# Optimization experiments

Hardware: AMD Instinct MI355X
Metric: run time of the kernel (lower is better)

Reference implementation:

```python
import jax, jax.numpy as jnp
import numpy as np

MAX_LEN = 128
VOCAB = 32000
SENTINEL = 2**30  # larger than any valid token id; pushes masked slots to the end after sort


def setup_inputs() -> dict:
    key = jax.random.key(0)
    k1, k2, k3, k4 = jax.random.split(key, 4)
    B, L = 262144, MAX_LEN
    input_ids = jax.random.randint(k1, (B, L), 0, VOCAB, dtype=jnp.int32)
    attention_mask = jax.random.randint(k2, (B, L), 0, 2, dtype=jnp.int32)
    # MLP params: Linear(3,32) -> ReLU -> Linear(32,32) -> ReLU
    W1 = jax.random.normal(k3, (3, 32), dtype=jnp.float32) * (1.0 / np.sqrt(3.0))
    b1 = jnp.zeros((32,), dtype=jnp.float32)
    W2 = jax.random.normal(k4, (32, 32), dtype=jnp.float32) * (1.0 / np.sqrt(32.0))
    b2 = jnp.zeros((32,), dtype=jnp.float32)
    return {"input_ids": input_ids, "attention_mask": attention_mask,
            "W1": W1, "b1": b1, "W2": W2, "b2": b2}


def _symbolic_feats(input_ids, attention_mask):
    # Batched replacement of the per-row torch.unique loop:
    # sort masked tokens per row, count boundaries between distinct values.
    mask = attention_mask.astype(bool)
    seq_len = jnp.sum(mask, axis=1)  # [B]
    ids_m = jnp.where(mask, input_ids, SENTINEL)  # masked-out slots -> sentinel
    s = jnp.sort(ids_m, axis=1)  # valid tokens first (ids < SENTINEL)
    valid = s < SENTINEL
    first = jnp.ones((s.shape[0], 1), dtype=bool)
    new_val = jnp.concatenate([first, s[:, 1:] != s[:, :-1]], axis=1)
    uniq = jnp.sum(valid & new_val, axis=1)  # [B] unique count among valid tokens
    seq_f = seq_len.astype(jnp.float32)
    uniq_f = uniq.astype(jnp.float32)
    uniq_ratio = jnp.where(seq_len > 0, uniq_f / jnp.maximum(seq_f, 1.0), 0.0)
    feats = jnp.stack([seq_f / MAX_LEN, uniq_f / MAX_LEN, uniq_ratio], axis=1)  # [B,3]
    return feats


def reference(input_ids, attention_mask, W1, b1, W2, b2):
    feats = _symbolic_feats(input_ids, attention_mask)  # [B,3]
    h = jax.nn.relu(feats @ W1 + b1)
    out = jax.nn.relu(h @ W2 + b2)
    return out
```

## Files before the change

kernel.cpp:

```cpp
#include <hip/hip_runtime.h>

#define ROW_LEN 128
#define NPAIR (129 * 129)
#define TBL 1024

__global__ __launch_bounds__(256) void mlp_table_kernel(
    const float* __restrict__ W1, const float* __restrict__ b1,
    const float* __restrict__ W2, const float* __restrict__ b2,
    float* __restrict__ table)
{
    const int tid = blockIdx.x * 256 + threadIdx.x;
    if (tid >= NPAIR * 32) return;
    const int p = tid >> 5;
    const int j = tid & 31;
    const int seq  = p / 129;
    const int uniq = p % 129;
    const float f0 = (float)seq  * (1.0f / 128.0f);
    const float f1 = (float)uniq * (1.0f / 128.0f);
    const float f2 = (seq > 0) ? ((float)uniq / (float)seq) : 0.0f;

    float acc = b2[j];
    #pragma unroll
    for (int jj = 0; jj < 32; ++jj) {
        float h = b1[jj];
        h = fmaf(f0, W1[jj],      h);
        h = fmaf(f1, W1[32 + jj], h);
        h = fmaf(f2, W1[64 + jj], h);
        h = fmaxf(h, 0.0f);
        acc = fmaf(h, W2[jj * 32 + j], acc);
    }
    table[tid] = fmaxf(acc, 0.0f);
}

__global__ __launch_bounds__(256) void rows_kernel(
    const int* __restrict__ ids, const int* __restrict__ amask,
    const float* __restrict__ table, float* __restrict__ out, int B)
{
    __shared__ unsigned tb[4][TBL];

    const int wave = threadIdx.x >> 6;
    const int lane = threadIdx.x & 63;
    const long row = (long)blockIdx.x * 4 + wave;
    if (row >= B) return;

    const long v = row * 64 + lane;
    const int2 id2 = ((const int2*)ids)[v];
    const int2 mk2 = ((const int2*)amask)[v];

    volatile unsigned* t = tb[wave];

    const bool mx = (mk2.x != 0);
    const bool my = (mk2.y != 0);
    const unsigned hx = ((unsigned)id2.x) & (TBL - 1);
    const unsigned hy = ((unsigned)id2.y) & (TBL - 1);

    if (mx) t[hx] = (unsigned)lane;
    if (my) t[hy] = (unsigned)(64 + lane);

    const unsigned r0 = t[hx];
    const unsigned r1 = t[hy];

    const bool win0 = mx && (r0 == (unsigned)lane);
    const bool win1 = my && (r1 == (unsigned)(64 + lane));

    const int seq = __popcll(__ballot(mx)) + __popcll(__ballot(my));
    int uniq = __popcll(__ballot(win0)) + __popcll(__ballot(win1));

    unsigned long long p0 = __ballot(mx && !win0);
    unsigned long long p1 = __ballot(my && !win1);
    while (p0 | p1) {
        int T;
        if (p0) {
            const int l = __ffsll((long long)p0) - 1;
            T = __builtin_amdgcn_readlane(id2.x, l);
        } else {
            const int l = __ffsll((long long)p1) - 1;
            T = __builtin_amdgcn_readlane(id2.y, l);
        }
        const unsigned long long ex = __ballot(mx && (id2.x == T));
        const unsigned long long ey = __ballot(my && (id2.y == T));
        const unsigned long long w  = __ballot((win0 && (id2.x == T)) ||
                                               (win1 && (id2.y == T)));
        uniq += (w == 0ull);
        p0 &= ~ex;
        p1 &= ~ey;
    }

    const int p = seq * 129 + uniq;
    if (lane < 32) out[row * 32 + lane] = table[p * 32 + lane];
}

extern "C" void kernel_launch(void* const* d_in, const int* in_sizes, int n_in,
                              void* d_out, int out_size, void* d_ws, size_t ws_size,
                              hipStream_t stream) {
    const int*   ids   = (const int*)d_in[0];
    const int*   amask = (const int*)d_in[1];
    const float* W1    = (const float*)d_in[2];
    const float* b1    = (const float*)d_in[3];
    const float* W2    = (const float*)d_in[4];
    const float* b2    = (const float*)d_in[5];
    float* out   = (float*)d_out;
    float* table = (float*)d_ws;

    const int B = in_sizes[0] / ROW_LEN;

    const int tblThreads = NPAIR * 32;
    mlp_table_kernel<<<(tblThreads + 255) / 256, 256, 0, stream>>>(W1, b1, W2, b2, table);

    rows_kernel<<<(B + 3) / 4, 256, 0, stream>>>(ids, amask, table, out, B);
}
```

Measured before the change: 287.9 us.

## Use LDS bitmap with atomicOr for dedup and nontemporal loads/stores

Replaces the per-wave 1024-entry last-writer hash table with a 1024-bit bitmap in LDS. An atomicOr on each token's bit tells that lane whether it was first, which shrinks LDS use and removes the write-then-read-back pass. Input loads and output stores become nontemporal because the data is streamed once. Collisions in the 10-bit bitmap are resolved by the existing exact ballot loop. Removing the volatile and adding LDS atomics may change latency, and the bitmap clear has no explicit barrier, relying on lockstep execution within a wave.

```diff
diff --git a/kernel.cpp b/kernel.cpp
--- a/kernel.cpp
+++ b/kernel.cpp
@@ -2,7 +2,8 @@
 
 #define ROW_LEN 128
 #define NPAIR (129 * 129)
-#define TBL 1024
+
+typedef int v2i __attribute__((ext_vector_type(2)));
 
 __global__ __launch_bounds__(256) void mlp_table_kernel(
     const float* __restrict__ W1, const float* __restrict__ b1,
@@ -36,7 +37,7 @@
     const int* __restrict__ ids, const int* __restrict__ amask,
     const float* __restrict__ table, float* __restrict__ out, int B)
 {
-    __shared__ unsigned tb[4][TBL];
+    __shared__ unsigned bm[4][32];
 
     const int wave = threadIdx.x >> 6;
     const int lane = threadIdx.x & 63;
@@ -44,50 +45,48 @@
     if (row >= B) return;
 
     const long v = row * 64 + lane;
-    const int2 id2 = ((const int2*)ids)[v];
-    const int2 mk2 = ((const int2*)amask)[v];
+    const v2i id2 = __builtin_nontemporal_load((const v2i*)ids + v);
+    const v2i mk2 = __builtin_nontemporal_load((const v2i*)amask + v);
 
-    volatile unsigned* t = tb[wave];
+    unsigned* t = bm[wave];
+    if (lane < 32) t[lane] = 0u;
 
     const bool mx = (mk2.x != 0);
     const bool my = (mk2.y != 0);
-    const unsigned hx = ((unsigned)id2.x) & (TBL - 1);
-    const unsigned hy = ((unsigned)id2.y) & (TBL - 1);
+    const unsigned tx = (unsigned)id2.x;
+    const unsigned ty = (unsigned)id2.y;
 
-    if (mx) t[hx] = (unsigned)lane;
-    if (my) t[hy] = (unsigned)(64 + lane);
-
-    const unsigned r0 = t[hx];
-    const unsigned r1 = t[hy];
-
-    const bool win0 = mx && (r0 == (unsigned)lane);
-    const bool win1 = my && (r1 == (unsigned)(64 + lane));
+    int h0 = 0, h1 = 0;
+    if (mx) {
+        const unsigned m = 1u << (tx & 31u);
+        h0 = ((atomicOr(&t[(tx >> 5) & 31u], m) & m) == 0u);
+    }
+    if (my) {
+        const unsigned m = 1u << (ty & 31u);
+        h1 = ((atomicOr(&t[(ty >> 5) & 31u], m) & m) == 0u);
+    }
 
     const int seq = __popcll(__ballot(mx)) + __popcll(__ballot(my));
-    int uniq = __popcll(__ballot(win0)) + __popcll(__ballot(win1));
+    int uniq = __popcll(__ballot(h0)) + __popcll(__ballot(h1));
 
-    unsigned long long p0 = __ballot(mx && !win0);
-    unsigned long long p1 = __ballot(my && !win1);
+    unsigned long long p0 = __ballot(mx && !h0);
+    unsigned long long p1 = __ballot(my && !h1);
     while (p0 | p1) {
         int T;
-        if (p0) {
-            const int l = __ffsll((long long)p0) - 1;
-            T = __builtin_amdgcn_readlane(id2.x, l);
-        } else {
-            const int l = __ffsll((long long)p1) - 1;
-            T = __builtin_amdgcn_readlane(id2.y, l);
-        }
-        const unsigned long long ex = __ballot(mx && (id2.x == T));
-        const unsigned long long ey = __ballot(my && (id2.y == T));
-        const unsigned long long w  = __ballot((win0 && (id2.x == T)) ||
-                                               (win1 && (id2.y == T)));
+        if (p0) T = __builtin_amdgcn_readlane(id2.x, __ffsll((long long)p0) - 1);
+        else    T = __builtin_amdgcn_readlane(id2.y, __ffsll((long long)p1) - 1);
+        const unsigned long long w =
+            __ballot((h0 && id2.x == T) || (h1 && id2.y == T));
         uniq += (w == 0ull);
-        p0 &= ~ex;
-        p1 &= ~ey;
+        p0 &= ~__ballot(id2.x == T);
+        p1 &= ~__ballot(id2.y == T);
     }
 
     const int p = seq * 129 + uniq;
-    if (lane < 32) out[row * 32 + lane] = table[p * 32 + lane];
+    if (lane < 32) {
+        const float r = table[p * 32 + lane];
+        __builtin_nontemporal_store(r, out + row * 32 + lane);
+    }
 }
 
 extern "C" void kernel_launch(void* const* d_in, const int* in_sizes, int n_in,
```

New measurement: 289.3 us. About the same (+0.5%).
